# Kernel optimization log

Measured on AMD Instinct MI355X. Metric: run time of the kernel, lower is better.

The kernel has to match this reference:

```python
import jax, jax.numpy as jnp
import numpy as np
import math

D_MODEL = 1024
N_HEADS = 16
D_K = D_MODEL // N_HEADS


def setup_inputs() -> dict:
    key = jax.random.key(0)
    ks = jax.random.split(key, 5)
    std = math.sqrt(2.0 / (D_MODEL + D_MODEL))
    x = jax.random.normal(ks[0], (2, 2048, D_MODEL), dtype=jnp.float32)
    W_q = jax.random.normal(ks[1], (D_MODEL, D_MODEL), dtype=jnp.float32) * std
    W_k = jax.random.normal(ks[2], (D_MODEL, D_MODEL), dtype=jnp.float32) * std
    W_v = jax.random.normal(ks[3], (D_MODEL, D_MODEL), dtype=jnp.float32) * std
    W_o = jax.random.normal(ks[4], (D_MODEL, D_MODEL), dtype=jnp.float32) * std
    return {"x": x, "W_q": W_q, "W_k": W_k, "W_v": W_v, "W_o": W_o}


def reference(x, W_q, W_k, W_v, W_o):
    B, S, D = x.shape
    H, dk = N_HEADS, D_K
    # projections: (B,S,D) @ (D,D)
    def split_heads(t):  # (B,S,D) -> (B,H,S,dk)
        return t.reshape(B, S, H, dk).transpose(0, 2, 1, 3)
    Q = split_heads(x @ W_q)
    K = split_heads(x @ W_k)
    V = split_heads(x @ W_v)
    scale = 1.0 / math.sqrt(dk)
    scores = jnp.einsum("bhqd,bhkd->bhqk", Q, K) * scale  # (B,H,S,S)
    attn = jax.nn.softmax(scores, axis=-1)
    out = jnp.einsum("bhqk,bhkd->bhqd", attn, V)  # (B,H,S,dk)
    concat = out.transpose(0, 2, 1, 3).reshape(B, S, D)
    return concat @ W_o
```

## Files before the change

### kernel.cpp

```cpp
#include <hip/hip_runtime.h>
#include <hip/hip_bf16.h>
#include <math.h>

#define DMODEL 1024
#define NHEADS 16
#define DKH    64
#define BATCH  2
#define SEQ    2048
#define MROWS  (BATCH * SEQ)
#define LOG2E  1.4426950408889634f

typedef __bf16 bf16_t;
typedef bf16_t bf16x8 __attribute__((ext_vector_type(8)));
typedef bf16_t bf16x4 __attribute__((ext_vector_type(4)));
typedef float  floatx4 __attribute__((ext_vector_type(4)));

__device__ __forceinline__ void glds16(const bf16_t* g, bf16_t* l) {
    __builtin_amdgcn_global_load_lds((__attribute__((address_space(1))) unsigned*)(g),
                                     (__attribute__((address_space(3))) unsigned*)(l),
                                     16, 0, 0);
}

__global__ void prep_kernel(const float* __restrict__ x,
                            const float* __restrict__ W0, const float* __restrict__ W1,
                            const float* __restrict__ W2, const float* __restrict__ W3,
                            bf16_t* __restrict__ xb, bf16_t* __restrict__ Wt) {
    __shared__ float t[32][33];
    int bx = blockIdx.x, by = blockIdx.y, z = blockIdx.z;
    int tx = threadIdx.x, ty = threadIdx.y;
    if (z == 0) {
        int tid = ty * 32 + tx;
#pragma unroll
        for (int k = 0; k < 4; ++k) {
            int slot = k * 256 + tid;
            int row = by * 128 + (slot >> 3);
            int col = bx * 32 + (slot & 7) * 4;
            float4 v = *(const float4*)&x[(size_t)row * DMODEL + col];
            bf16x4 o = {(bf16_t)v.x, (bf16_t)v.y, (bf16_t)v.z, (bf16_t)v.w};
            *(bf16x4*)&xb[(size_t)row * DMODEL + col] = o;
        }
        return;
    }
    const float* W = (z == 1) ? W0 : (z == 2) ? W1 : (z == 3) ? W2 : W3;
    bf16_t* dst = Wt + (size_t)(z - 1) * DMODEL * DMODEL;
#pragma unroll
    for (int i = 0; i < 32; i += 8)
        t[ty + i][tx] = W[(size_t)(by * 32 + ty + i) * DMODEL + bx * 32 + tx];
    __syncthreads();
#pragma unroll
    for (int i = 0; i < 32; i += 8)
        dst[(size_t)(bx * 32 + ty + i) * DMODEL + by * 32 + tx] = (bf16_t)t[tx][ty + i];
}

__global__ __launch_bounds__(256) void gemm_qkv_kernel(const bf16_t* __restrict__ A,
                                                       const bf16_t* __restrict__ Bt,
                                                       bf16_t* __restrict__ Qfb,
                                                       bf16_t* __restrict__ Kfb,
                                                       bf16_t* __restrict__ Vfb) {
    __shared__ bf16_t sm[16384];
    bf16_t* As = sm;
    bf16_t* Bs = sm + 8192;
    int tid = threadIdx.x;
    int w = tid >> 6, l = tid & 63, g = l >> 4, lm = l & 15;
    int wr = w >> 1, wc = w & 1;
    int m0 = blockIdx.y * 128, n0 = blockIdx.x * 128;
    int r8 = l >> 3, s8 = l & 7, cw = s8 ^ r8;

    floatx4 acc[4][4];
#pragma unroll
    for (int i = 0; i < 4; ++i)
#pragma unroll
        for (int j = 0; j < 4; ++j) { floatx4 z = {0.f, 0.f, 0.f, 0.f}; acc[i][j] = z; }

    const bf16_t* Ag = A  + (size_t)(m0 + w * 32 + r8) * DMODEL + cw * 8;
    const bf16_t* Bg = Bt + (size_t)(n0 + w * 32 + r8) * DMODEL + cw * 8;

    for (int k0 = 0; k0 < DMODEL; k0 += 64) {
        __syncthreads();
#pragma unroll
        for (int j = 0; j < 4; ++j) {
            glds16(Ag + (size_t)j * 8 * DMODEL + k0, &As[(w * 32 + j * 8) * 64]);
            glds16(Bg + (size_t)j * 8 * DMODEL + k0, &Bs[(w * 32 + j * 8) * 64]);
        }
        __syncthreads();
#pragma unroll
        for (int kk = 0; kk < 2; ++kk) {
            bf16x8 af[4], bfr[4];
            int c = kk * 4 + g;
            int sw = (c ^ (lm & 7)) * 8;
#pragma unroll
            for (int i = 0; i < 4; ++i) {
                af[i]  = *(const bf16x8*)&As[(wr * 64 + i * 16 + lm) * 64 + sw];
                bfr[i] = *(const bf16x8*)&Bs[(wc * 64 + i * 16 + lm) * 64 + sw];
            }
#pragma unroll
            for (int i = 0; i < 4; ++i)
#pragma unroll
                for (int j = 0; j < 4; ++j)
                    acc[i][j] = __builtin_amdgcn_mfma_f32_16x16x32_bf16(af[i], bfr[j], acc[i][j], 0, 0, 0);
        }
    }

    __syncthreads();
    int mat = n0 >> 10;
    int headb = (n0 & 1023) >> 6;
    int b = m0 >> 11;
    int ktb = (m0 & 2047) >> 6;
    float scale = (mat == 0) ? (0.125f * LOG2E) : 1.0f;

    if (mat <= 1) {
#pragma unroll
        for (int i = 0; i < 4; ++i)
#pragma unroll
            for (int j = 0; j < 4; ++j) {
                int d = j * 16 + lm;
                int base = (wc * 2 + wr) * 4096 + (i * 2 + (d >> 5)) * 512 + ((d >> 3) & 3) * 128 + (d & 7);
#pragma unroll
                for (int r = 0; r < 4; ++r)
                    sm[base + (g * 4 + r) * 8] = (bf16_t)(acc[i][j][r] * scale);
            }
    } else {
#pragma unroll
        for (int i = 0; i < 4; ++i)
#pragma unroll
            for (int j = 0; j < 4; ++j) {
                int base = (wc * 2 + wr) * 4096 + (j * 2 + (i >> 1)) * 512 +
                           (((i & 1) * 2 + (g >> 1)) * 16 + lm) * 8 + (g & 1) * 4;
                bf16x4 pk = {(bf16_t)acc[i][j][0], (bf16_t)acc[i][j][1],
                             (bf16_t)acc[i][j][2], (bf16_t)acc[i][j][3]};
                *(bf16x4*)&sm[base] = pk;
            }
    }
    __syncthreads();
    bf16_t* outbuf = (mat == 0) ? Qfb : (mat == 1) ? Kfb : Vfb;
#pragma unroll
    for (int rep = 0; rep < 8; ++rep) {
        int idx = rep * 256 + tid;
        int c = idx >> 9;
        int off = (idx & 511) * 8;
        int bh2 = b * NHEADS + headb + (c >> 1);
        int kt = ktb + (c & 1);
        *(bf16x8*)(outbuf + ((size_t)bh2 * 32 + kt) * 4096 + off) = *(const bf16x8*)&sm[c * 4096 + off];
    }
}

__global__ __launch_bounds__(256) void gemmO_kernel(const bf16_t* __restrict__ A,
                                                    const bf16_t* __restrict__ Bt,
                                                    float* __restrict__ outp) {
    __shared__ bf16_t As[64 * 64];
    __shared__ bf16_t Bs[128 * 64];
    int tid = threadIdx.x;
    int w = tid >> 6, l = tid & 63, g = l >> 4, lm = l & 15;
    int wr = w & 1, wc = w >> 1;
    int m0 = blockIdx.y * 64, n0 = blockIdx.x * 128;
    int r8 = l >> 3, s8 = l & 7, cw = s8 ^ r8;

    floatx4 acc[2][4];
#pragma unroll
    for (int i = 0; i < 2; ++i)
#pragma unroll
        for (int j = 0; j < 4; ++j) { floatx4 z = {0.f, 0.f, 0.f, 0.f}; acc[i][j] = z; }

    const bf16_t* Ag = A  + (size_t)(m0 + w * 16 + r8) * DMODEL + cw * 8;
    const bf16_t* Bg = Bt + (size_t)(n0 + w * 32 + r8) * DMODEL + cw * 8;

    for (int k0 = 0; k0 < DMODEL; k0 += 64) {
        __syncthreads();
#pragma unroll
        for (int j = 0; j < 2; ++j)
            glds16(Ag + (size_t)j * 8 * DMODEL + k0, &As[(w * 16 + j * 8) * 64]);
#pragma unroll
        for (int j = 0; j < 4; ++j)
            glds16(Bg + (size_t)j * 8 * DMODEL + k0, &Bs[(w * 32 + j * 8) * 64]);
        __syncthreads();
#pragma unroll
        for (int kk = 0; kk < 2; ++kk) {
            bf16x8 af[2], bfr[4];
            int c = kk * 4 + g;
            int sw = (c ^ (lm & 7)) * 8;
#pragma unroll
            for (int i = 0; i < 2; ++i)
                af[i] = *(const bf16x8*)&As[(wr * 32 + i * 16 + lm) * 64 + sw];
#pragma unroll
            for (int j = 0; j < 4; ++j)
                bfr[j] = *(const bf16x8*)&Bs[(wc * 64 + j * 16 + lm) * 64 + sw];
#pragma unroll
            for (int i = 0; i < 2; ++i)
#pragma unroll
                for (int j = 0; j < 4; ++j)
                    acc[i][j] = __builtin_amdgcn_mfma_f32_16x16x32_bf16(af[i], bfr[j], acc[i][j], 0, 0, 0);
        }
    }

#pragma unroll
    for (int i = 0; i < 2; ++i)
#pragma unroll
        for (int j = 0; j < 4; ++j) {
            int nc = n0 + wc * 64 + j * 16 + lm;
            int mb = m0 + wr * 32 + i * 16 + g * 4;
#pragma unroll
            for (int r = 0; r < 4; ++r)
                outp[(size_t)(mb + r) * DMODEL + nc] = acc[i][j][r];
        }
}

__global__ __launch_bounds__(256, 2) void attn_kernel(const bf16_t* __restrict__ Qf,
                                                      const bf16_t* __restrict__ Kf,
                                                      const bf16_t* __restrict__ Vf,
                                                      bf16_t* __restrict__ Cc) {
    __shared__ __align__(16) char smem[43008];
    bf16_t* Ps   = (bf16_t*)smem;
    float*  Mbuf = (float*)smem;
    float*  Lbuf = (float*)(smem + 36864);
    bf16_t* Ct   = (bf16_t*)(smem + 37888);

    int tid = threadIdx.x;
    int w = tid >> 6, l = tid & 63, g = l >> 4, lm = l & 15;
    int bh = blockIdx.x, b = bh >> 4, h = bh & 15;
    int q0 = blockIdx.y * 64;

    const bf16_t* Qfh = Qf + ((size_t)bh * 32 + (q0 >> 6)) * 4096 + l * 8;
    const bf16_t* Kfh = Kf + (size_t)bh * 32 * 4096 + l * 8;
    const bf16_t* Vfh = Vf + (size_t)bh * 32 * 4096 + l * 8;

    bf16x8 qf[4][2];
#pragma unroll
    for (int nt = 0; nt < 4; ++nt)
#pragma unroll
        for (int kk = 0; kk < 2; ++kk)
            qf[nt][kk] = *(const bf16x8*)(Qfh + (nt * 2 + kk) * 512);

    floatx4 oacc[4][4];
#pragma unroll
    for (int dt = 0; dt < 4; ++dt)
#pragma unroll
        for (int nt = 0; nt < 4; ++nt) { floatx4 z = {0.f, 0.f, 0.f, 0.f}; oacc[dt][nt] = z; }
    float lsum[4] = {0.f, 0.f, 0.f, 0.f};

    int kt0 = w * 8;
    bf16x8 kfa[2][2], kfb[2][2], vfa[4], vfb[4];
    {
        const bf16_t* Kb0 = Kfh + (size_t)kt0 * 4096;
#pragma unroll
        for (int m2 = 0; m2 < 2; ++m2)
#pragma unroll
            for (int kk = 0; kk < 2; ++kk)
                kfa[m2][kk] = *(const bf16x8*)(Kb0 + (m2 * 2 + kk) * 512);
    }

    for (int it = 0; it < 8; ++it) {
        const bf16_t* Tb = Kfh + (size_t)(kt0 + it) * 4096;
        const bf16_t* Vb = Vfh + (size_t)(kt0 + it) * 4096;
        const bf16_t* Tn = Kfh + (size_t)(kt0 + ((it < 7) ? it + 1 : 0)) * 4096;

#pragma unroll
        for (int dt = 0; dt < 4; ++dt) vfa[dt] = *(const bf16x8*)(Vb + (dt * 2 + 0) * 512);
#pragma unroll
        for (int m2 = 0; m2 < 2; ++m2)
#pragma unroll
            for (int kk = 0; kk < 2; ++kk)
                kfb[m2][kk] = *(const bf16x8*)(Tb + (4 + m2 * 2 + kk) * 512);

        floatx4 sa[2][4];
#pragma unroll
        for (int m2 = 0; m2 < 2; ++m2)
#pragma unroll
            for (int nt = 0; nt < 4; ++nt) { floatx4 z = {0.f, 0.f, 0.f, 0.f}; sa[m2][nt] = z; }
#pragma unroll
        for (int kk = 0; kk < 2; ++kk)
#pragma unroll
            for (int m2 = 0; m2 < 2; ++m2)
#pragma unroll
                for (int nt = 0; nt < 4; ++nt)
                    sa[m2][nt] = __builtin_amdgcn_mfma_f32_16x16x32_bf16(kfa[m2][kk], qf[nt][kk], sa[m2][nt], 0, 0, 0);

#pragma unroll
        for (int dt = 0; dt < 4; ++dt) vfb[dt] = *(const bf16x8*)(Vb + (dt * 2 + 1) * 512);
#pragma unroll
        for (int m2 = 0; m2 < 2; ++m2)
#pragma unroll
            for (int kk = 0; kk < 2; ++kk)
                kfa[m2][kk] = *(const bf16x8*)(Tn + (m2 * 2 + kk) * 512);

        floatx4 sb[2][4];
#pragma unroll
        for (int m2 = 0; m2 < 2; ++m2)
#pragma unroll
            for (int nt = 0; nt < 4; ++nt) { floatx4 z = {0.f, 0.f, 0.f, 0.f}; sb[m2][nt] = z; }
#pragma unroll
        for (int kk = 0; kk < 2; ++kk)
#pragma unroll
            for (int m2 = 0; m2 < 2; ++m2)
#pragma unroll
                for (int nt = 0; nt < 4; ++nt)
                    sb[m2][nt] = __builtin_amdgcn_mfma_f32_16x16x32_bf16(kfb[m2][kk], qf[nt][kk], sb[m2][nt], 0, 0, 0);

#pragma unroll
        for (int m2 = 0; m2 < 2; ++m2)
#pragma unroll
            for (int nt = 0; nt < 4; ++nt) {
                float p0 = __builtin_amdgcn_exp2f(sa[m2][nt][0]);
                float p1 = __builtin_amdgcn_exp2f(sa[m2][nt][1]);
                float p2 = __builtin_amdgcn_exp2f(sa[m2][nt][2]);
                float p3 = __builtin_amdgcn_exp2f(sa[m2][nt][3]);
                lsum[nt] += (p0 + p1) + (p2 + p3);
                bf16x4 pk = {(bf16_t)p0, (bf16_t)p1, (bf16_t)p2, (bf16_t)p3};
                *(bf16x4*)&Ps[w * 2560 + (nt * 16 + lm) * 40 + m2 * 16 + g * 4] = pk;
            }
        {
            bf16x8 bp[4];
#pragma unroll
            for (int nt = 0; nt < 4; ++nt)
                bp[nt] = *(const bf16x8*)&Ps[w * 2560 + (nt * 16 + lm) * 40 + g * 8];
#pragma unroll
            for (int dt = 0; dt < 4; ++dt)
#pragma unroll
                for (int nt = 0; nt < 4; ++nt)
                    oacc[dt][nt] = __builtin_amdgcn_mfma_f32_16x16x32_bf16(vfa[dt], bp[nt], oacc[dt][nt], 0, 0, 0);
        }

#pragma unroll
        for (int m2 = 0; m2 < 2; ++m2)
#pragma unroll
            for (int nt = 0; nt < 4; ++nt) {
                float p0 = __builtin_amdgcn_exp2f(sb[m2][nt][0]);
                float p1 = __builtin_amdgcn_exp2f(sb[m2][nt][1]);
                float p2 = __builtin_amdgcn_exp2f(sb[m2][nt][2]);
                float p3 = __builtin_amdgcn_exp2f(sb[m2][nt][3]);
                lsum[nt] += (p0 + p1) + (p2 + p3);
                bf16x4 pk = {(bf16_t)p0, (bf16_t)p1, (bf16_t)p2, (bf16_t)p3};
                *(bf16x4*)&Ps[w * 2560 + (nt * 16 + lm) * 40 + m2 * 16 + g * 4] = pk;
            }
        {
            bf16x8 bp[4];
#pragma unroll
            for (int nt = 0; nt < 4; ++nt)
                bp[nt] = *(const bf16x8*)&Ps[w * 2560 + (nt * 16 + lm) * 40 + g * 8];
#pragma unroll
            for (int dt = 0; dt < 4; ++dt)
#pragma unroll
                for (int nt = 0; nt < 4; ++nt)
                    oacc[dt][nt] = __builtin_amdgcn_mfma_f32_16x16x32_bf16(vfb[dt], bp[nt], oacc[dt][nt], 0, 0, 0);
        }
    }

#pragma unroll
    for (int nt = 0; nt < 4; ++nt) {
        float s = lsum[nt];
        s += __shfl_xor(s, 16, 64);
        s += __shfl_xor(s, 32, 64);
        lsum[nt] = s;
    }

    float linv = 0.f;
#pragma unroll
    for (int p = 0; p < 2; ++p) {
        __syncthreads();
#pragma unroll
        for (int dh = 0; dh < 2; ++dh) {
            int dt = p * 2 + dh;
#pragma unroll
            for (int nt = 0; nt < 4; ++nt)
                *(floatx4*)&Mbuf[w * 2304 + (nt * 16 + lm) * 36 + dh * 16 + g * 4] = oacc[dt][nt];
        }
        if (p == 0 && g == 0)
#pragma unroll
            for (int nt = 0; nt < 4; ++nt)
                Lbuf[w * 64 + nt * 16 + lm] = lsum[nt];
        __syncthreads();
        if (p == 0) {
            float lt = 0.f;
#pragma unroll
            for (int w2 = 0; w2 < 4; ++w2)
                lt += Lbuf[w2 * 64 + w * 16 + lm];
            linv = 1.0f / lt;
        }
#pragma unroll
        for (int cc = 0; cc < 2; ++cc) {
            floatx4 s = {0.f, 0.f, 0.f, 0.f};
#pragma unroll
            for (int w2 = 0; w2 < 4; ++w2)
                s += *(const floatx4*)&Mbuf[w2 * 2304 + (w * 16 + lm) * 36 + cc * 16 + g * 4];
            bf16x4 pk = {(bf16_t)(s[0] * linv), (bf16_t)(s[1] * linv),
                         (bf16_t)(s[2] * linv), (bf16_t)(s[3] * linv)};
            *(bf16x4*)&Ct[w * 640 + lm * 40 + cc * 16 + g * 4] = pk;
        }
        {
            int row = l >> 2, dp = l & 3;
            bf16x8 v = *(const bf16x8*)&Ct[w * 640 + row * 40 + dp * 8];
            *(bf16x8*)&Cc[((size_t)(b * SEQ + q0 + w * 16 + row)) * DMODEL + h * DKH + p * 32 + dp * 8] = v;
        }
    }
}

extern "C" void kernel_launch(void* const* d_in, const int* in_sizes, int n_in,
                              void* d_out, int out_size, void* d_ws, size_t ws_size,
                              hipStream_t stream) {
    const float* x  = (const float*)d_in[0];
    const float* Wq = (const float*)d_in[1];
    const float* Wk = (const float*)d_in[2];
    const float* Wv = (const float*)d_in[3];
    const float* Wo = (const float*)d_in[4];

    const size_t NX = (size_t)MROWS * DMODEL;
    const size_t NW = (size_t)DMODEL * DMODEL;
    bf16_t* ws  = (bf16_t*)d_ws;
    bf16_t* xb  = ws;
    bf16_t* Wt  = xb + NX;
    bf16_t* Wto = Wt + 3 * NW;
    bf16_t* Qfb = Wt + 4 * NW;
    bf16_t* Kfb = Qfb + NX;
    bf16_t* Vfb = Kfb + NX;
    bf16_t* Cc  = Vfb + NX;

    prep_kernel<<<dim3(32, 32, 5), dim3(32, 8), 0, stream>>>(x, Wq, Wk, Wv, Wo, xb, Wt);

    gemm_qkv_kernel<<<dim3(3 * DMODEL / 128, MROWS / 128), 256, 0, stream>>>(xb, Wt, Qfb, Kfb, Vfb);

    attn_kernel<<<dim3(BATCH * NHEADS, SEQ / 64), 256, 0, stream>>>(Qfb, Kfb, Vfb, Cc);

    gemmO_kernel<<<dim3(DMODEL / 128, MROWS / 64), 256, 0, stream>>>(Cc, Wto, (float*)d_out);
}
```

Measured before the change: 175.7 us.

## Split attention waves 2x2 over queries and keys to shrink LDS and raise occupancy

Each block's four waves are regrouped into two query-row groups times two key halves. Previously each wave covered all 64 queries over one quarter of the keys. Per-wave accumulators and score tiles shrink, and so do the P staging buffer and the cross-wave reduction buffer. Total LDS falls from about 42KB to about 26KB, and launch bounds ask for 3 blocks per CU. The final reduction now combines only two partials with a single sync pair. In exchange each wave reloads K/V tiles over twice as many iterations, so K/V traffic per block doubles relative to the MFMA work.

Measured after the change: 187.2 us. 6.6% more time.

```diff
diff --git a/kernel.cpp b/kernel.cpp
--- a/kernel.cpp
+++ b/kernel.cpp
@@ -204,18 +204,19 @@
         }
 }
 
-__global__ __launch_bounds__(256, 2) void attn_kernel(const bf16_t* __restrict__ Qf,
+__global__ __launch_bounds__(256, 3) void attn_kernel(const bf16_t* __restrict__ Qf,
                                                       const bf16_t* __restrict__ Kf,
                                                       const bf16_t* __restrict__ Vf,
                                                       bf16_t* __restrict__ Cc) {
-    __shared__ __align__(16) char smem[43008];
+    __shared__ __align__(16) char smem[26880];
     bf16_t* Ps   = (bf16_t*)smem;
     float*  Mbuf = (float*)smem;
-    float*  Lbuf = (float*)(smem + 36864);
-    bf16_t* Ct   = (bf16_t*)(smem + 37888);
+    float*  Lbuf = (float*)(smem + 17408);
+    bf16_t* Ct   = (bf16_t*)(smem + 17664);
 
     int tid = threadIdx.x;
     int w = tid >> 6, l = tid & 63, g = l >> 4, lm = l & 15;
+    int qw = w >> 1, ks = w & 1;
     int bh = blockIdx.x, b = bh >> 4, h = bh & 15;
     int q0 = blockIdx.y * 64;
 
@@ -223,21 +224,21 @@
     const bf16_t* Kfh = Kf + (size_t)bh * 32 * 4096 + l * 8;
     const bf16_t* Vfh = Vf + (size_t)bh * 32 * 4096 + l * 8;
 
-    bf16x8 qf[4][2];
-#pragma unroll
-    for (int nt = 0; nt < 4; ++nt)
+    bf16x8 qf[2][2];
+#pragma unroll
+    for (int nt = 0; nt < 2; ++nt)
 #pragma unroll
         for (int kk = 0; kk < 2; ++kk)
-            qf[nt][kk] = *(const bf16x8*)(Qfh + (nt * 2 + kk) * 512);
-
-    floatx4 oacc[4][4];
+            qf[nt][kk] = *(const bf16x8*)(Qfh + (qw * 4 + nt * 2 + kk) * 512);
+
+    floatx4 oacc[4][2];
 #pragma unroll
     for (int dt = 0; dt < 4; ++dt)
 #pragma unroll
-        for (int nt = 0; nt < 4; ++nt) { floatx4 z = {0.f, 0.f, 0.f, 0.f}; oacc[dt][nt] = z; }
-    float lsum[4] = {0.f, 0.f, 0.f, 0.f};
-
-    int kt0 = w * 8;
+        for (int nt = 0; nt < 2; ++nt) { floatx4 z = {0.f, 0.f, 0.f, 0.f}; oacc[dt][nt] = z; }
+    float lsum[2] = {0.f, 0.f};
+
+    int kt0 = ks * 16;
     bf16x8 kfa[2][2], kfb[2][2], vfa[4], vfb[4];
     {
         const bf16_t* Kb0 = Kfh + (size_t)kt0 * 4096;
@@ -248,10 +249,10 @@
                 kfa[m2][kk] = *(const bf16x8*)(Kb0 + (m2 * 2 + kk) * 512);
     }
 
-    for (int it = 0; it < 8; ++it) {
+    for (int it = 0; it < 16; ++it) {
         const bf16_t* Tb = Kfh + (size_t)(kt0 + it) * 4096;
         const bf16_t* Vb = Vfh + (size_t)(kt0 + it) * 4096;
-        const bf16_t* Tn = Kfh + (size_t)(kt0 + ((it < 7) ? it + 1 : 0)) * 4096;
+        const bf16_t* Tn = Kfh + (size_t)(kt0 + ((it < 15) ? it + 1 : 0)) * 4096;
 
 #pragma unroll
         for (int dt = 0; dt < 4; ++dt) vfa[dt] = *(const bf16x8*)(Vb + (dt * 2 + 0) * 512);
@@ -261,17 +262,17 @@
             for (int kk = 0; kk < 2; ++kk)
                 kfb[m2][kk] = *(const bf16x8*)(Tb + (4 + m2 * 2 + kk) * 512);
 
-        floatx4 sa[2][4];
-#pragma unroll
-        for (int m2 = 0; m2 < 2; ++m2)
-#pragma unroll
-            for (int nt = 0; nt < 4; ++nt) { floatx4 z = {0.f, 0.f, 0.f, 0.f}; sa[m2][nt] = z; }
+        floatx4 sa[2][2];
+#pragma unroll
+        for (int m2 = 0; m2 < 2; ++m2)
+#pragma unroll
+            for (int nt = 0; nt < 2; ++nt) { floatx4 z = {0.f, 0.f, 0.f, 0.f}; sa[m2][nt] = z; }
 #pragma unroll
         for (int kk = 0; kk < 2; ++kk)
 #pragma unroll
             for (int m2 = 0; m2 < 2; ++m2)
 #pragma unroll
-                for (int nt = 0; nt < 4; ++nt)
+                for (int nt = 0; nt < 2; ++nt)
                     sa[m2][nt] = __builtin_amdgcn_mfma_f32_16x16x32_bf16(kfa[m2][kk], qf[nt][kk], sa[m2][nt], 0, 0, 0);
 
 #pragma unroll
@@ -282,113 +283,111 @@
             for (int kk = 0; kk < 2; ++kk)
                 kfa[m2][kk] = *(const bf16x8*)(Tn + (m2 * 2 + kk) * 512);
 
-        floatx4 sb[2][4];
-#pragma unroll
-        for (int m2 = 0; m2 < 2; ++m2)
-#pragma unroll
-            for (int nt = 0; nt < 4; ++nt) { floatx4 z = {0.f, 0.f, 0.f, 0.f}; sb[m2][nt] = z; }
+        floatx4 sb[2][2];
+#pragma unroll
+        for (int m2 = 0; m2 < 2; ++m2)
+#pragma unroll
+            for (int nt = 0; nt < 2; ++nt) { floatx4 z = {0.f, 0.f, 0.f, 0.f}; sb[m2][nt] = z; }
 #pragma unroll
         for (int kk = 0; kk < 2; ++kk)
 #pragma unroll
             for (int m2 = 0; m2 < 2; ++m2)
 #pragma unroll
-                for (int nt = 0; nt < 4; ++nt)
+                for (int nt = 0; nt < 2; ++nt)
                     sb[m2][nt] = __builtin_amdgcn_mfma_f32_16x16x32_bf16(kfb[m2][kk], qf[nt][kk], sb[m2][nt], 0, 0, 0);
 
 #pragma unroll
         for (int m2 = 0; m2 < 2; ++m2)
 #pragma unroll
-            for (int nt = 0; nt < 4; ++nt) {
+            for (int nt = 0; nt < 2; ++nt) {
                 float p0 = __builtin_amdgcn_exp2f(sa[m2][nt][0]);
                 float p1 = __builtin_amdgcn_exp2f(sa[m2][nt][1]);
                 float p2 = __builtin_amdgcn_exp2f(sa[m2][nt][2]);
                 float p3 = __builtin_amdgcn_exp2f(sa[m2][nt][3]);
                 lsum[nt] += (p0 + p1) + (p2 + p3);
                 bf16x4 pk = {(bf16_t)p0, (bf16_t)p1, (bf16_t)p2, (bf16_t)p3};
-                *(bf16x4*)&Ps[w * 2560 + (nt * 16 + lm) * 40 + m2 * 16 + g * 4] = pk;
+                *(bf16x4*)&Ps[w * 1280 + (nt * 16 + lm) * 40 + m2 * 16 + g * 4] = pk;
             }
         {
-            bf16x8 bp[4];
-#pragma unroll
-            for (int nt = 0; nt < 4; ++nt)
-                bp[nt] = *(const bf16x8*)&Ps[w * 2560 + (nt * 16 + lm) * 40 + g * 8];
+            bf16x8 bp[2];
+#pragma unroll
+            for (int nt = 0; nt < 2; ++nt)
+                bp[nt] = *(const bf16x8*)&Ps[w * 1280 + (nt * 16 + lm) * 40 + g * 8];
 #pragma unroll
             for (int dt = 0; dt < 4; ++dt)
 #pragma unroll
-                for (int nt = 0; nt < 4; ++nt)
+                for (int nt = 0; nt < 2; ++nt)
                     oacc[dt][nt] = __builtin_amdgcn_mfma_f32_16x16x32_bf16(vfa[dt], bp[nt], oacc[dt][nt], 0, 0, 0);
         }
 
 #pragma unroll
         for (int m2 = 0; m2 < 2; ++m2)
 #pragma unroll
-            for (int nt = 0; nt < 4; ++nt) {
+            for (int nt = 0; nt < 2; ++nt) {
                 float p0 = __builtin_amdgcn_exp2f(sb[m2][nt][0]);
                 float p1 = __builtin_amdgcn_exp2f(sb[m2][nt][1]);
                 float p2 = __builtin_amdgcn_exp2f(sb[m2][nt][2]);
                 float p3 = __builtin_amdgcn_exp2f(sb[m2][nt][3]);
                 lsum[nt] += (p0 + p1) + (p2 + p3);
                 bf16x4 pk = {(bf16_t)p0, (bf16_t)p1, (bf16_t)p2, (bf16_t)p3};
-                *(bf16x4*)&Ps[w * 2560 + (nt * 16 + lm) * 40 + m2 * 16 + g * 4] = pk;
+                *(bf16x4*)&Ps[w * 1280 + (nt * 16 + lm) * 40 + m2 * 16 + g * 4] = pk;
             }
         {
-            bf16x8 bp[4];
-#pragma unroll
-            for (int nt = 0; nt < 4; ++nt)
-                bp[nt] = *(const bf16x8*)&Ps[w * 2560 + (nt * 16 + lm) * 40 + g * 8];
+            bf16x8 bp[2];
+#pragma unroll
+            for (int nt = 0; nt < 2; ++nt)
+                bp[nt] = *(const bf16x8*)&Ps[w * 1280 + (nt * 16 + lm) * 40 + g * 8];
 #pragma unroll
             for (int dt = 0; dt < 4; ++dt)
 #pragma unroll
-                for (int nt = 0; nt < 4; ++nt)
+                for (int nt = 0; nt < 2; ++nt)
                     oacc[dt][nt] = __builtin_amdgcn_mfma_f32_16x16x32_bf16(vfb[dt], bp[nt], oacc[dt][nt], 0, 0, 0);
         }
     }
 
 #pragma unroll
-    for (int nt = 0; nt < 4; ++nt) {
+    for (int nt = 0; nt < 2; ++nt) {
         float s = lsum[nt];
         s += __shfl_xor(s, 16, 64);
         s += __shfl_xor(s, 32, 64);
         lsum[nt] = s;
     }
 
-    float linv = 0.f;
-#pragma unroll
-    for (int p = 0; p < 2; ++p) {
-        __syncthreads();
-#pragma unroll
-        for (int dh = 0; dh < 2; ++dh) {
-            int dt = p * 2 + dh;
-#pragma unroll
-            for (int nt = 0; nt < 4; ++nt)
-                *(floatx4*)&Mbuf[w * 2304 + (nt * 16 + lm) * 36 + dh * 16 + g * 4] = oacc[dt][nt];
-        }
-        if (p == 0 && g == 0)
-#pragma unroll
-            for (int nt = 0; nt < 4; ++nt)
-                Lbuf[w * 64 + nt * 16 + lm] = lsum[nt];
-        __syncthreads();
-        if (p == 0) {
-            float lt = 0.f;
-#pragma unroll
-            for (int w2 = 0; w2 < 4; ++w2)
-                lt += Lbuf[w2 * 64 + w * 16 + lm];
-            linv = 1.0f / lt;
-        }
-#pragma unroll
-        for (int cc = 0; cc < 2; ++cc) {
-            floatx4 s = {0.f, 0.f, 0.f, 0.f};
-#pragma unroll
-            for (int w2 = 0; w2 < 4; ++w2)
-                s += *(const floatx4*)&Mbuf[w2 * 2304 + (w * 16 + lm) * 36 + cc * 16 + g * 4];
-            bf16x4 pk = {(bf16_t)(s[0] * linv), (bf16_t)(s[1] * linv),
-                         (bf16_t)(s[2] * linv), (bf16_t)(s[3] * linv)};
-            *(bf16x4*)&Ct[w * 640 + lm * 40 + cc * 16 + g * 4] = pk;
-        }
-        {
-            int row = l >> 2, dp = l & 3;
-            bf16x8 v = *(const bf16x8*)&Ct[w * 640 + row * 40 + dp * 8];
-            *(bf16x8*)&Cc[((size_t)(b * SEQ + q0 + w * 16 + row)) * DMODEL + h * DKH + p * 32 + dp * 8] = v;
+    __syncthreads();
+    if (ks == 1) {
+#pragma unroll
+        for (int dt = 0; dt < 4; ++dt)
+#pragma unroll
+            for (int nt = 0; nt < 2; ++nt)
+                *(floatx4*)&Mbuf[qw * 2176 + (nt * 16 + lm) * 68 + dt * 16 + g * 4] = oacc[dt][nt];
+        if (g == 0)
+#pragma unroll
+            for (int nt = 0; nt < 2; ++nt)
+                Lbuf[qw * 32 + nt * 16 + lm] = lsum[nt];
+    }
+    __syncthreads();
+    if (ks == 0) {
+        float linv[2];
+#pragma unroll
+        for (int nt = 0; nt < 2; ++nt)
+            linv[nt] = 1.0f / (lsum[nt] + Lbuf[qw * 32 + nt * 16 + lm]);
+#pragma unroll
+        for (int dt = 0; dt < 4; ++dt)
+#pragma unroll
+            for (int nt = 0; nt < 2; ++nt) {
+                floatx4 part = *(const floatx4*)&Mbuf[qw * 2176 + (nt * 16 + lm) * 68 + dt * 16 + g * 4];
+                bf16x4 pk = {(bf16_t)((oacc[dt][nt][0] + part[0]) * linv[nt]),
+                             (bf16_t)((oacc[dt][nt][1] + part[1]) * linv[nt]),
+                             (bf16_t)((oacc[dt][nt][2] + part[2]) * linv[nt]),
+                             (bf16_t)((oacc[dt][nt][3] + part[3]) * linv[nt])};
+                *(bf16x4*)&Ct[qw * 2304 + (nt * 16 + lm) * 72 + dt * 16 + g * 4] = pk;
+            }
+#pragma unroll
+        for (int rep = 0; rep < 4; ++rep) {
+            int idx = rep * 64 + l;
+            int row = idx >> 3, dp = idx & 7;
+            bf16x8 v = *(const bf16x8*)&Ct[qw * 2304 + row * 72 + dp * 8];
+            *(bf16x8*)&Cc[((size_t)(b * SEQ + q0 + qw * 32 + row)) * DMODEL + h * DKH + dp * 8] = v;
         }
     }
 }
```
